# Optimization experiments

Measured on AMD Instinct MI355X. Metric: run time of the kernel, lower is better.

Reference implementation:

```python
import jax, jax.numpy as jnp
import numpy as np

B, L, D, H = 2, 2048, 1024, 16
DH = D // H


def setup_inputs() -> dict:
    key = jax.random.key(0)
    ks = jax.random.split(key, 5)
    bound = 1.0 / D ** 0.5
    x = jax.random.normal(ks[0], (B, L, D), dtype=jnp.float32)
    # causal mask: 0 means masked out
    mask = jnp.tril(jnp.ones((L, L), dtype=jnp.int32))[None].repeat(B, axis=0)
    Wq = jax.random.uniform(ks[1], (D, D), jnp.float32, -bound, bound)
    Wk = jax.random.uniform(ks[2], (D, D), jnp.float32, -bound, bound)
    Wv = jax.random.uniform(ks[3], (D, D), jnp.float32, -bound, bound)
    Wo = jax.random.uniform(ks[4], (D, D), jnp.float32, -bound, bound)
    return {"x": x, "mask": mask, "Wq": Wq, "Wk": Wk, "Wv": Wv, "Wo": Wo}


def _split_heads(t):
    # (B, L, D) -> (B, H, L, DH)
    b, l, _ = t.shape
    return t.reshape(b, l, H, DH).transpose(0, 2, 1, 3)


def reference(x, mask, Wq, Wk, Wv, Wo):
    # projections: torch Linear does x @ W.T with W:(out,in)
    q = _split_heads(x @ Wq.T)  # (B,H,L,DH)
    k = _split_heads(x @ Wk.T)
    v = _split_heads(x @ Wv.T)
    scores = jnp.einsum('bhqd,bhkd->bhqk', q, k) / jnp.sqrt(jnp.float32(DH))
    m = mask[:, None, :, :]  # (B,1,L,L)
    scores = jnp.where(m == 0, jnp.float32(-jnp.inf), scores)
    attn = jax.nn.softmax(scores, axis=-1)
    out = jnp.einsum('bhqk,bhkd->bhqd', attn, v)  # (B,H,L,DH)
    out = out.transpose(0, 2, 1, 3).reshape(x.shape[0], x.shape[1], D)
    return out @ Wo.T
```

## Files before the change

kernel.cpp:

```cpp
#include <hip/hip_runtime.h>
#include <stdint.h>


typedef unsigned short u16;
typedef __attribute__((ext_vector_type(8))) short short8;
typedef __attribute__((ext_vector_type(4))) float f32x4;
typedef __attribute__((ext_vector_type(4))) unsigned int uint4v;

#define NEG_BIG (-1e30f)
#define QSCALE 0.18033688011112042f

__device__ __forceinline__ f32x4 mfma16(short8 a, short8 b, f32x4 c) {
    return __builtin_amdgcn_mfma_f32_16x16x32_bf16(a, b, c, 0, 0, 0);
}

__device__ __forceinline__ u16 f2bf(float f) {
    uint32_t u = __float_as_uint(f);
    u += 0x7fffu + ((u >> 16) & 1u);
    return (u16)(u >> 16);
}

#if __has_builtin(__builtin_amdgcn_cvt_pk_bf16_f32)
__device__ __forceinline__ unsigned int f2bf_pk(float a, float b) {
    return __builtin_bit_cast(unsigned int, __builtin_amdgcn_cvt_pk_bf16_f32(a, b));
}
#else
__device__ __forceinline__ unsigned int f2bf_pk(float a, float b) {
    return (unsigned int)f2bf(a) | ((unsigned int)f2bf(b) << 16);
}
#endif

__device__ __forceinline__ void load_lds_16B(const u16* g, u16* lds_base) {
    __builtin_amdgcn_global_load_lds(
        (__attribute__((address_space(1))) void*)(uintptr_t)(const void*)g,
        (__attribute__((address_space(3))) void*)lds_base,
        16, 0, 0);
}

__global__ __launch_bounds__(256) void cvt_kernel(
    const float* __restrict__ x, const float* __restrict__ wq, const float* __restrict__ wk,
    const float* __restrict__ wv, const float* __restrict__ wo, u16* __restrict__ dst)
{
    const int gid = blockIdx.x * 256 + threadIdx.x;
    const float* src; size_t off;
    if (gid < 524288)      { src = x;  off = (size_t)gid * 8; }
    else if (gid < 655360) { src = wq; off = (size_t)(gid - 524288) * 8; }
    else if (gid < 786432) { src = wk; off = (size_t)(gid - 655360) * 8; }
    else if (gid < 917504) { src = wv; off = (size_t)(gid - 786432) * 8; }
    else                   { src = wo; off = (size_t)(gid - 917504) * 8; }
    float4 a = *(const float4*)(src + off);
    float4 b = *(const float4*)(src + off + 4);
    uint4v u = { f2bf_pk(a.x, a.y), f2bf_pk(a.z, a.w),
                 f2bf_pk(b.x, b.y), f2bf_pk(b.z, b.w) };
    *(uint4v*)(dst + (size_t)gid * 8) = u;
}

__device__ __forceinline__ void gemm_bt_128x128(
    const u16* __restrict__ A, const u16* __restrict__ Bw,
    u16* at, u16* bt, int m0, int n0, f32x4 acc[4][4])
{
    const int tid  = threadIdx.x;
    const int w    = tid >> 6, lane = tid & 63;
    const int quad = lane >> 4, l15 = lane & 15;
    const int wm   = (w >> 1) * 64, wn = (w & 1) * 64;
    const int srow0 = w * 32 + (lane >> 2);
    const int sp    = lane & 3;

    for (int k0 = 0; k0 < 1024; k0 += 32) {
#pragma unroll
        for (int c = 0; c < 2; ++c) {
            int row = srow0 + c * 16;
            int g   = sp ^ ((row >> 1) & 3);
            load_lds_16B(A  + (size_t)(m0 + row) * 1024 + k0 + g * 8, at + (w * 32 + c * 16) * 32);
            load_lds_16B(Bw + (size_t)(n0 + row) * 1024 + k0 + g * 8, bt + (w * 32 + c * 16) * 32);
        }
        __syncthreads();
        short8 af[4], bf[4];
#pragma unroll
        for (int rf = 0; rf < 4; ++rf) {
            int ra = wm + rf * 16 + l15, sa = quad ^ ((ra >> 1) & 3);
            af[rf] = *(const short8*)(at + ra * 32 + sa * 8);
            int rb = wn + rf * 16 + l15, sb = quad ^ ((rb >> 1) & 3);
            bf[rf] = *(const short8*)(bt + rb * 32 + sb * 8);
        }
#pragma unroll
        for (int rf = 0; rf < 4; ++rf)
#pragma unroll
            for (int cf = 0; cf < 4; ++cf)
                acc[rf][cf] = mfma16(af[rf], bf[cf], acc[rf][cf]);
        __syncthreads();
    }
}

__global__ __launch_bounds__(256, 3) void qkv_gemm(
    const u16* __restrict__ xb, const u16* __restrict__ Wq, const u16* __restrict__ Wk,
    const u16* __restrict__ Wv, u16* __restrict__ qbuf, u16* __restrict__ kbuf,
    u16* __restrict__ vtbuf)
{
    __shared__ __align__(16) u16 at[128 * 32];
    __shared__ __align__(16) u16 bt[128 * 32];
    const int m0  = blockIdx.x * 128;
    const int by  = blockIdx.y;
    const int sel = by >> 3;
    const int n0  = (by & 7) * 128;
    const u16* Wsel = sel == 0 ? Wq : (sel == 1 ? Wk : Wv);

    f32x4 acc[4][4];
    const f32x4 z = {0.f, 0.f, 0.f, 0.f};
#pragma unroll
    for (int i = 0; i < 4; ++i)
#pragma unroll
        for (int j = 0; j < 4; ++j) acc[i][j] = z;

    gemm_bt_128x128(xb, Wsel, at, bt, m0, n0, acc);

    const int tid  = threadIdx.x, w = tid >> 6, lane = tid & 63;
    const int quad = lane >> 4, l15 = lane & 15;
    const int wm   = (w >> 1) * 64, wn = (w & 1) * 64;

    if (sel < 2) {
        u16* dst = sel == 0 ? qbuf : kbuf;
        const float scl = sel == 0 ? QSCALE : 1.0f;
#pragma unroll
        for (int rf = 0; rf < 4; ++rf)
#pragma unroll
            for (int cf = 0; cf < 4; ++cf) {
                int n = n0 + wn + cf * 16 + l15;
                int h = n >> 6, dh = n & 63;
#pragma unroll
                for (int r = 0; r < 4; ++r) {
                    int m = m0 + wm + rf * 16 + quad * 4 + r;
                    int b = m >> 11, l = m & 2047;
                    dst[(((size_t)(b * 16 + h)) * 2048 + l) * 64 + dh] = f2bf(acc[rf][cf][r] * scl);
                }
            }
    } else {
#pragma unroll
        for (int rf = 0; rf < 4; ++rf)
#pragma unroll
            for (int cf = 0; cf < 4; ++cf) {
                int n = n0 + wn + cf * 16 + l15;
                int h = n >> 6, dh = n & 63;
                int m = m0 + wm + rf * 16 + quad * 4;
                int b = m >> 11, l = m & 2047;
                ushort4 pk;
                pk.x = f2bf(acc[rf][cf][0]);
                pk.y = f2bf(acc[rf][cf][1]);
                pk.z = f2bf(acc[rf][cf][2]);
                pk.w = f2bf(acc[rf][cf][3]);
                *(ushort4*)(vtbuf + (((size_t)(b * 16 + h)) * 64 + dh) * 2048 + l) = pk;
            }
    }
}

__global__ __launch_bounds__(256, 3) void attn_kernel(
    const u16* __restrict__ qbuf, const u16* __restrict__ kbuf,
    const u16* __restrict__ vtbuf, u16* __restrict__ attn)
{
    __shared__ __align__(16) u16 kt[2][64 * 64];
    __shared__ __align__(16) u16 vt[2][64 * 64];
    __shared__ __align__(16) u16 pt[4 * 32 * 64];

    const int tid  = threadIdx.x, w = tid >> 6, lane = tid & 63;
    const int quad = lane >> 4, l15 = lane & 15;
    const int bh   = blockIdx.y;
    const int jq   = (blockIdx.y & 16) ? (int)blockIdx.x : (15 - (int)blockIdx.x);
    const int q0   = jq * 128;
    const int qw   = q0 + w * 32;

    const u16* qbase = qbuf  + (size_t)bh * 2048 * 64;
    const u16* kbase = kbuf  + (size_t)bh * 2048 * 64;
    const u16* vbase = vtbuf + (size_t)bh * 64 * 2048;
    u16* pw = pt + w * (32 * 64);
    const int b = bh >> 4, h = bh & 15;

    const f32x4 z = {0.f, 0.f, 0.f, 0.f};

    short8 qf[2][2];
#pragma unroll
    for (int rf = 0; rf < 2; ++rf)
#pragma unroll
        for (int ks = 0; ks < 2; ++ks)
            qf[rf][ks] = *(const short8*)(qbase + (size_t)(qw + rf * 16 + l15) * 64 + ks * 32 + quad * 8);

    f32x4 o[2][4];
    float mrun[2], lrun[2];
#pragma unroll
    for (int rf = 0; rf < 2; ++rf) {
#pragma unroll
        for (int df = 0; df < 4; ++df) o[rf][df] = z;
        mrun[rf] = NEG_BIG; lrun[rf] = 0.f;
    }

    auto stage = [&](int t, int buf) {
        const int k0 = t * 64;
#pragma unroll
        for (int c = 0; c < 2; ++c) {
            int row = w * 16 + c * 8 + (lane >> 3);
            int g   = (lane & 7) ^ (row & 7);
            load_lds_16B(kbase + (size_t)(k0 + row) * 64 + g * 8, kt[buf] + (w * 16 + c * 8) * 64);
            load_lds_16B(vbase + (size_t)row * 2048 + k0 + g * 8, vt[buf] + (w * 16 + c * 8) * 64);
        }
    };

    const int ntiles = 2 * jq + 2;
    stage(0, 0);
    for (int t = 0; t < ntiles; ++t) {
        __syncthreads();
        if (t + 1 < ntiles) stage(t + 1, (t + 1) & 1);
        const int k0 = t * 64;
        if (k0 <= qw + 31) {
            const u16* ktb = kt[t & 1];
            const u16* vtb = vt[t & 1];
            f32x4 st[2][4];
#pragma unroll
            for (int rf = 0; rf < 2; ++rf)
#pragma unroll
                for (int nf = 0; nf < 4; ++nf) st[rf][nf] = z;
#pragma unroll
            for (int ks = 0; ks < 2; ++ks)
#pragma unroll
                for (int nf = 0; nf < 4; ++nf) {
                    int row = nf * 16 + l15;
                    int ph  = (ks * 4 + quad) ^ (row & 7);
                    short8 kf = *(const short8*)(ktb + row * 64 + ph * 8);
#pragma unroll
                    for (int rf = 0; rf < 2; ++rf)
                        st[rf][nf] = mfma16(kf, qf[rf][ks], st[rf][nf]);
                }
            if (k0 + 63 > qw) {
#pragma unroll
                for (int rf = 0; rf < 2; ++rf) {
                    int qrow = qw + rf * 16 + l15;
#pragma unroll
                    for (int nf = 0; nf < 4; ++nf)
#pragma unroll
                        for (int r = 0; r < 4; ++r) {
                            int key = k0 + nf * 16 + quad * 4 + r;
                            if (key > qrow) st[rf][nf][r] = NEG_BIG;
                        }
                }
            }
#pragma unroll
            for (int rf = 0; rf < 2; ++rf) {
                float mx = st[rf][0][0];
#pragma unroll
                for (int nf = 0; nf < 4; ++nf)
#pragma unroll
                    for (int r = 0; r < 4; ++r) mx = fmaxf(mx, st[rf][nf][r]);
                mx = fmaxf(mx, __shfl_xor(mx, 16));
                mx = fmaxf(mx, __shfl_xor(mx, 32));
                float mnew = fmaxf(mrun[rf], mx);
                float alpha = exp2f(mrun[rf] - mnew);
                float sum = 0.f;
#pragma unroll
                for (int nf = 0; nf < 4; ++nf)
#pragma unroll
                    for (int r = 0; r < 4; ++r) {
                        float p = exp2f(st[rf][nf][r] - mnew);
                        st[rf][nf][r] = p;
                        sum += p;
                    }
                sum += __shfl_xor(sum, 16);
                sum += __shfl_xor(sum, 32);
                lrun[rf] = lrun[rf] * alpha + sum;
                mrun[rf] = mnew;
#pragma unroll
                for (int df = 0; df < 4; ++df) o[rf][df] *= alpha;
            }
#pragma unroll
            for (int rf = 0; rf < 2; ++rf)
#pragma unroll
                for (int nf = 0; nf < 4; ++nf) {
                    int ph = (nf * 2 + (quad >> 1)) ^ (l15 & 7);
                    uint2 pk2;
                    pk2.x = f2bf_pk(st[rf][nf][0], st[rf][nf][1]);
                    pk2.y = f2bf_pk(st[rf][nf][2], st[rf][nf][3]);
                    *(uint2*)(pw + (rf * 16 + l15) * 64 + ph * 8 + (quad & 1) * 4) = pk2;
                }
#pragma unroll
            for (int ks2 = 0; ks2 < 2; ++ks2) {
                short8 pb[2];
#pragma unroll
                for (int rf = 0; rf < 2; ++rf) {
                    int ph = (ks2 * 4 + quad) ^ (l15 & 7);
                    pb[rf] = *(const short8*)(pw + (rf * 16 + l15) * 64 + ph * 8);
                }
#pragma unroll
                for (int df = 0; df < 4; ++df) {
                    int row = df * 16 + l15;
                    int ph  = (ks2 * 4 + quad) ^ (row & 7);
                    short8 vf = *(const short8*)(vtb + row * 64 + ph * 8);
#pragma unroll
                    for (int rf = 0; rf < 2; ++rf)
                        o[rf][df] = mfma16(vf, pb[rf], o[rf][df]);
                }
            }
        }
    }

#pragma unroll
    for (int rf = 0; rf < 2; ++rf) {
        float inv = 1.f / lrun[rf];
        int qrow = qw + rf * 16 + l15;
        u16* obase = attn + ((size_t)(b * 2048 + qrow)) * 1024 + h * 64;
#pragma unroll
        for (int df = 0; df < 4; ++df)
#pragma unroll
            for (int r = 0; r < 4; ++r) {
                int dh = df * 16 + quad * 4 + r;
                obase[dh] = f2bf(o[rf][df][r] * inv);
            }
    }
}

__global__ __launch_bounds__(256, 3) void oproj_gemm(
    const u16* __restrict__ attn, const u16* __restrict__ Wo, float* __restrict__ out)
{
    __shared__ __align__(16) u16 at[128 * 32];
    __shared__ __align__(16) u16 bt[128 * 32];
    const int m0 = blockIdx.x * 128;
    const int n0 = blockIdx.y * 128;

    f32x4 acc[4][4];
    const f32x4 z = {0.f, 0.f, 0.f, 0.f};
#pragma unroll
    for (int i = 0; i < 4; ++i)
#pragma unroll
        for (int j = 0; j < 4; ++j) acc[i][j] = z;

    gemm_bt_128x128(attn, Wo, at, bt, m0, n0, acc);

    const int tid  = threadIdx.x, w = tid >> 6, lane = tid & 63;
    const int quad = lane >> 4, l15 = lane & 15;
    const int wm   = (w >> 1) * 64, wn = (w & 1) * 64;
#pragma unroll
    for (int rf = 0; rf < 4; ++rf)
#pragma unroll
        for (int cf = 0; cf < 4; ++cf) {
            int n = n0 + wn + cf * 16 + l15;
#pragma unroll
            for (int r = 0; r < 4; ++r) {
                int m = m0 + wm + rf * 16 + quad * 4 + r;
                out[(size_t)m * 1024 + n] = acc[rf][cf][r];
            }
        }
}

extern "C" void kernel_launch(void* const* d_in, const int* in_sizes, int n_in,
                              void* d_out, int out_size, void* d_ws, size_t ws_size,
                              hipStream_t stream) {
    const float* x  = (const float*)d_in[0];
    const float* Wq = (const float*)d_in[2];
    const float* Wk = (const float*)d_in[3];
    const float* Wv = (const float*)d_in[4];
    const float* Wo = (const float*)d_in[5];

    u16* ws    = (u16*)d_ws;
    const size_t M = 1024 * 1024;
    u16* qbuf  = ws;
    u16* kbuf  = ws + 4 * M;
    u16* vtb   = ws + 8 * M;
    u16* attnb = ws + 12 * M;
    u16* cvtb  = ws + 16 * M;
    u16* xb    = cvtb;
    u16* wqb   = cvtb + 4 * M;
    u16* wkb   = cvtb + 5 * M;
    u16* wvb   = cvtb + 6 * M;
    u16* wob   = cvtb + 7 * M;
    float* out = (float*)d_out;

    cvt_kernel<<<4096, 256, 0, stream>>>(x, Wq, Wk, Wv, Wo, cvtb);
    qkv_gemm<<<dim3(32, 24), 256, 0, stream>>>(xb, wqb, wkb, wvb, qbuf, kbuf, vtb);
    attn_kernel<<<dim3(16, 32), 256, 0, stream>>>(qbuf, kbuf, vtb, attnb);
    oproj_gemm<<<dim3(32, 8), 256, 0, stream>>>(attnb, wob, out);
}
```

Measured before the change: 218.6 us.

## Split attention block across 8 waves with 16 query rows each

The attention kernel now launches 512 threads (8 waves) per block, and each wave handles 16 query rows instead of 32. K/V staging is spread over the 8 waves and the per-wave P scratch shrinks. This gives more waves per block for latency hiding and lower register pressure per wave. In exchange, each K/V fragment read from LDS feeds half as many MFMAs, so LDS traffic per unit of compute doubles.

```diff
diff --git a/kernel.cpp b/kernel.cpp
--- a/kernel.cpp
+++ b/kernel.cpp
@@ -153,54 +153,45 @@
     }
 }
 
-__global__ __launch_bounds__(256, 3) void attn_kernel(
+__global__ __launch_bounds__(512, 4) void attn_kernel(
     const u16* __restrict__ qbuf, const u16* __restrict__ kbuf,
     const u16* __restrict__ vtbuf, u16* __restrict__ attn)
 {
     __shared__ __align__(16) u16 kt[2][64 * 64];
     __shared__ __align__(16) u16 vt[2][64 * 64];
-    __shared__ __align__(16) u16 pt[4 * 32 * 64];
+    __shared__ __align__(16) u16 pt[8 * 16 * 64];
 
     const int tid  = threadIdx.x, w = tid >> 6, lane = tid & 63;
     const int quad = lane >> 4, l15 = lane & 15;
     const int bh   = blockIdx.y;
     const int jq   = (blockIdx.y & 16) ? (int)blockIdx.x : (15 - (int)blockIdx.x);
     const int q0   = jq * 128;
-    const int qw   = q0 + w * 32;
+    const int qw   = q0 + w * 16;
 
     const u16* qbase = qbuf  + (size_t)bh * 2048 * 64;
     const u16* kbase = kbuf  + (size_t)bh * 2048 * 64;
     const u16* vbase = vtbuf + (size_t)bh * 64 * 2048;
-    u16* pw = pt + w * (32 * 64);
+    u16* pw = pt + w * (16 * 64);
     const int b = bh >> 4, h = bh & 15;
 
     const f32x4 z = {0.f, 0.f, 0.f, 0.f};
 
-    short8 qf[2][2];
-#pragma unroll
-    for (int rf = 0; rf < 2; ++rf)
-#pragma unroll
-        for (int ks = 0; ks < 2; ++ks)
-            qf[rf][ks] = *(const short8*)(qbase + (size_t)(qw + rf * 16 + l15) * 64 + ks * 32 + quad * 8);
-
-    f32x4 o[2][4];
-    float mrun[2], lrun[2];
-#pragma unroll
-    for (int rf = 0; rf < 2; ++rf) {
-#pragma unroll
-        for (int df = 0; df < 4; ++df) o[rf][df] = z;
-        mrun[rf] = NEG_BIG; lrun[rf] = 0.f;
-    }
+    short8 qf[2];
+#pragma unroll
+    for (int ks = 0; ks < 2; ++ks)
+        qf[ks] = *(const short8*)(qbase + (size_t)(qw + l15) * 64 + ks * 32 + quad * 8);
+
+    f32x4 o[4];
+    float mrun = NEG_BIG, lrun = 0.f;
+#pragma unroll
+    for (int df = 0; df < 4; ++df) o[df] = z;
 
     auto stage = [&](int t, int buf) {
         const int k0 = t * 64;
-#pragma unroll
-        for (int c = 0; c < 2; ++c) {
-            int row = w * 16 + c * 8 + (lane >> 3);
-            int g   = (lane & 7) ^ (row & 7);
-            load_lds_16B(kbase + (size_t)(k0 + row) * 64 + g * 8, kt[buf] + (w * 16 + c * 8) * 64);
-            load_lds_16B(vbase + (size_t)row * 2048 + k0 + g * 8, vt[buf] + (w * 16 + c * 8) * 64);
-        }
+        int row = w * 8 + (lane >> 3);
+        int g   = (lane & 7) ^ (row & 7);
+        load_lds_16B(kbase + (size_t)(k0 + row) * 64 + g * 8, kt[buf] + (w * 8) * 64);
+        load_lds_16B(vbase + (size_t)row * 2048 + k0 + g * 8, vt[buf] + (w * 8) * 64);
     };
 
     const int ntiles = 2 * jq + 2;
@@ -209,14 +200,12 @@
         __syncthreads();
         if (t + 1 < ntiles) stage(t + 1, (t + 1) & 1);
         const int k0 = t * 64;
-        if (k0 <= qw + 31) {
+        if (k0 <= qw + 15) {
             const u16* ktb = kt[t & 1];
             const u16* vtb = vt[t & 1];
-            f32x4 st[2][4];
-#pragma unroll
-            for (int rf = 0; rf < 2; ++rf)
-#pragma unroll
-                for (int nf = 0; nf < 4; ++nf) st[rf][nf] = z;
+            f32x4 st[4];
+#pragma unroll
+            for (int nf = 0; nf < 4; ++nf) st[nf] = z;
 #pragma unroll
             for (int ks = 0; ks < 2; ++ks)
 #pragma unroll
@@ -224,92 +213,77 @@
                     int row = nf * 16 + l15;
                     int ph  = (ks * 4 + quad) ^ (row & 7);
                     short8 kf = *(const short8*)(ktb + row * 64 + ph * 8);
-#pragma unroll
-                    for (int rf = 0; rf < 2; ++rf)
-                        st[rf][nf] = mfma16(kf, qf[rf][ks], st[rf][nf]);
+                    st[nf] = mfma16(kf, qf[ks], st[nf]);
                 }
             if (k0 + 63 > qw) {
-#pragma unroll
-                for (int rf = 0; rf < 2; ++rf) {
-                    int qrow = qw + rf * 16 + l15;
-#pragma unroll
-                    for (int nf = 0; nf < 4; ++nf)
-#pragma unroll
-                        for (int r = 0; r < 4; ++r) {
-                            int key = k0 + nf * 16 + quad * 4 + r;
-                            if (key > qrow) st[rf][nf][r] = NEG_BIG;
-                        }
-                }
-            }
-#pragma unroll
-            for (int rf = 0; rf < 2; ++rf) {
-                float mx = st[rf][0][0];
+                int qrow = qw + l15;
 #pragma unroll
                 for (int nf = 0; nf < 4; ++nf)
 #pragma unroll
-                    for (int r = 0; r < 4; ++r) mx = fmaxf(mx, st[rf][nf][r]);
+                    for (int r = 0; r < 4; ++r) {
+                        int key = k0 + nf * 16 + quad * 4 + r;
+                        if (key > qrow) st[nf][r] = NEG_BIG;
+                    }
+            }
+            {
+                float mx = st[0][0];
+#pragma unroll
+                for (int nf = 0; nf < 4; ++nf)
+#pragma unroll
+                    for (int r = 0; r < 4; ++r) mx = fmaxf(mx, st[nf][r]);
                 mx = fmaxf(mx, __shfl_xor(mx, 16));
                 mx = fmaxf(mx, __shfl_xor(mx, 32));
-                float mnew = fmaxf(mrun[rf], mx);
-                float alpha = exp2f(mrun[rf] - mnew);
+                float mnew = fmaxf(mrun, mx);
+                float alpha = exp2f(mrun - mnew);
                 float sum = 0.f;
 #pragma unroll
                 for (int nf = 0; nf < 4; ++nf)
 #pragma unroll
                     for (int r = 0; r < 4; ++r) {
-                        float p = exp2f(st[rf][nf][r] - mnew);
-                        st[rf][nf][r] = p;
+                        float p = exp2f(st[nf][r] - mnew);
+                        st[nf][r] = p;
                         sum += p;
                     }
                 sum += __shfl_xor(sum, 16);
                 sum += __shfl_xor(sum, 32);
-                lrun[rf] = lrun[rf] * alpha + sum;
-                mrun[rf] = mnew;
-#pragma unroll
-                for (int df = 0; df < 4; ++df) o[rf][df] *= alpha;
-            }
-#pragma unroll
-            for (int rf = 0; rf < 2; ++rf)
-#pragma unroll
-                for (int nf = 0; nf < 4; ++nf) {
-                    int ph = (nf * 2 + (quad >> 1)) ^ (l15 & 7);
-                    uint2 pk2;
-                    pk2.x = f2bf_pk(st[rf][nf][0], st[rf][nf][1]);
-                    pk2.y = f2bf_pk(st[rf][nf][2], st[rf][nf][3]);
-                    *(uint2*)(pw + (rf * 16 + l15) * 64 + ph * 8 + (quad & 1) * 4) = pk2;
-                }
+                lrun = lrun * alpha + sum;
+                mrun = mnew;
+#pragma unroll
+                for (int df = 0; df < 4; ++df) o[df] *= alpha;
+            }
+#pragma unroll
+            for (int nf = 0; nf < 4; ++nf) {
+                int ph = (nf * 2 + (quad >> 1)) ^ (l15 & 7);
+                uint2 pk2;
+                pk2.x = f2bf_pk(st[nf][0], st[nf][1]);
+                pk2.y = f2bf_pk(st[nf][2], st[nf][3]);
+                *(uint2*)(pw + l15 * 64 + ph * 8 + (quad & 1) * 4) = pk2;
+            }
 #pragma unroll
             for (int ks2 = 0; ks2 < 2; ++ks2) {
-                short8 pb[2];
-#pragma unroll
-                for (int rf = 0; rf < 2; ++rf) {
-                    int ph = (ks2 * 4 + quad) ^ (l15 & 7);
-                    pb[rf] = *(const short8*)(pw + (rf * 16 + l15) * 64 + ph * 8);
-                }
+                int phb = (ks2 * 4 + quad) ^ (l15 & 7);
+                short8 pb = *(const short8*)(pw + l15 * 64 + phb * 8);
 #pragma unroll
                 for (int df = 0; df < 4; ++df) {
                     int row = df * 16 + l15;
                     int ph  = (ks2 * 4 + quad) ^ (row & 7);
                     short8 vf = *(const short8*)(vtb + row * 64 + ph * 8);
-#pragma unroll
-                    for (int rf = 0; rf < 2; ++rf)
-                        o[rf][df] = mfma16(vf, pb[rf], o[rf][df]);
+                    o[df] = mfma16(vf, pb, o[df]);
                 }
             }
         }
     }
 
-#pragma unroll
-    for (int rf = 0; rf < 2; ++rf) {
-        float inv = 1.f / lrun[rf];
-        int qrow = qw + rf * 16 + l15;
+    {
+        float inv = 1.f / lrun;
+        int qrow = qw + l15;
         u16* obase = attn + ((size_t)(b * 2048 + qrow)) * 1024 + h * 64;
 #pragma unroll
         for (int df = 0; df < 4; ++df)
 #pragma unroll
             for (int r = 0; r < 4; ++r) {
                 int dh = df * 16 + quad * 4 + r;
-                obase[dh] = f2bf(o[rf][df][r] * inv);
+                obase[dh] = f2bf(o[df][r] * inv);
             }
     }
 }
@@ -372,6 +346,6 @@
 
     cvt_kernel<<<4096, 256, 0, stream>>>(x, Wq, Wk, Wv, Wo, cvtb);
     qkv_gemm<<<dim3(32, 24), 256, 0, stream>>>(xb, wqb, wkb, wvb, qbuf, kbuf, vtb);
-    attn_kernel<<<dim3(16, 32), 256, 0, stream>>>(qbuf, kbuf, vtb, attnb);
+    attn_kernel<<<dim3(16, 32), 512, 0, stream>>>(qbuf, kbuf, vtb, attnb);
     oproj_gemm<<<dim3(32, 8), 256, 0, stream>>>(attnb, wob, out);
 }
```

New measurement: 210.5 us. 3.7% less time.
